# Kernel tuning notes

Measured on AMD Instinct MI355X. Metric: run time of the kernel, lower is better.

Reference implementation:

```python
import jax, jax.numpy as jnp
import numpy as np

H = 128  # GRU units / embedding dim


def gru_dir(x, mask, W, U, b):
    """Keras GRU (reset_after=True), return final state.
    x: [B,T,D] float, mask: [B,T] bool, W: [D,3H], U: [H,3H], b: [2,3H] (input/recurrent bias).
    Gate order in kernels: z, r, h (Keras convention).
    """
    bi, bh = b[0], b[1]
    xproj = jnp.einsum('btd,dk->btk', x, W) + bi          # [B,T,3H] precomputed input projection
    xproj_t = jnp.transpose(xproj, (1, 0, 2))             # [T,B,3H]
    mask_t = jnp.transpose(mask, (1, 0))                  # [T,B]
    h0 = jnp.zeros((x.shape[0], H), dtype=x.dtype)

    def step(h, inp):
        xp, m = inp                                       # [B,3H], [B]
        hU = h @ U + bh                                   # [B,3H]
        z = jax.nn.sigmoid(xp[:, :H] + hU[:, :H])
        r = jax.nn.sigmoid(xp[:, H:2 * H] + hU[:, H:2 * H])
        hh = jnp.tanh(xp[:, 2 * H:] + r * hU[:, 2 * H:])
        h_new = z * h + (1.0 - z) * hh
        h = jnp.where(m[:, None], h_new, h)               # masked steps carry state
        return h, None

    h_final, _ = jax.lax.scan(step, h0, (xproj_t, mask_t))
    return h_final                                        # [B,H]


def setup_inputs() -> dict:
    key = jax.random.key(0)
    ks = jax.random.split(key, 10)
    B, T, V = 512, 512, 50000
    tokens = jax.random.randint(ks[0], (B, T), 0, V, dtype=jnp.int32)
    s = 0.05
    emb = jax.random.normal(ks[1], (V, H), dtype=jnp.float32) * s
    Wf = jax.random.normal(ks[2], (H, 3 * H), dtype=jnp.float32) * s
    Uf = jax.random.normal(ks[3], (H, 3 * H), dtype=jnp.float32) * s
    bf = jnp.zeros((2, 3 * H), dtype=jnp.float32)
    Wb = jax.random.normal(ks[4], (H, 3 * H), dtype=jnp.float32) * s
    Ub = jax.random.normal(ks[5], (H, 3 * H), dtype=jnp.float32) * s
    bb = jnp.zeros((2, 3 * H), dtype=jnp.float32)
    Wd = jax.random.normal(ks[6], (2 * H, 1), dtype=jnp.float32) * s
    bd = jnp.zeros((1,), dtype=jnp.float32)
    return {"tokens": tokens, "emb": emb, "Wf": Wf, "Uf": Uf, "bf": bf,
            "Wb": Wb, "Ub": Ub, "bb": bb, "Wd": Wd, "bd": bd}


def reference(tokens, emb, Wf, Uf, bf, Wb, Ub, bb, Wd, bd):
    x = emb[tokens]                                       # [B,T,H] embedding lookup
    mask = jnp.any(x != 0.0, axis=-1)                     # Masking(mask_value=0)
    x = x * mask[..., None].astype(x.dtype)               # Masking zeroes masked steps
    h_fwd = gru_dir(x, mask, Wf, Uf, bf)                  # forward direction
    h_bwd = gru_dir(x[:, ::-1, :], mask[:, ::-1], Wb, Ub, bb)  # backward direction (reversed time)
    h = jnp.concatenate([h_fwd, h_bwd], axis=-1)          # [B,2H] concat merge
    return jax.nn.sigmoid(h @ Wd + bd)                    # [B,1]
```

## Files before the change

### kernel.cpp

```cpp
#include <hip/hip_runtime.h>

#define TLEN 512
#define HD 128
#define VOC 50000

typedef float fvec4 __attribute__((ext_vector_type(4)));
typedef int   ivec4 __attribute__((ext_vector_type(4)));
typedef int   ivec8 __attribute__((ext_vector_type(8)));

__device__ __forceinline__ float fsig(float a){
  return __builtin_amdgcn_rcpf(1.f + __builtin_amdgcn_exp2f(-1.44269504f * a));
}

__global__ void emb_cvt8(const float* __restrict__ emb, int* __restrict__ out, int n4){
  int i = blockIdx.x * blockDim.x + threadIdx.x;
  if (i < n4){
    float4 v = *(const float4*)(emb + (size_t)i * 4);
    int p = __builtin_amdgcn_cvt_pk_fp8_f32(16.f * v.x, 16.f * v.y, 0, 0);
    p     = __builtin_amdgcn_cvt_pk_fp8_f32(16.f * v.z, 16.f * v.w, p, 1);
    out[i] = p;
  }
}

__global__ __launch_bounds__(512, 2) void gru_scan(
    const int* __restrict__ tokens, const unsigned char* __restrict__ embq,
    const float* __restrict__ Wf, const float* __restrict__ Uf, const float* __restrict__ bfv,
    const float* __restrict__ Wb, const float* __restrict__ Ub, const float* __restrict__ bbv,
    float* __restrict__ hbuf)
{
  const int tid  = threadIdx.x;
  const int wid  = tid >> 6, lane = tid & 63;
  const int l15  = lane & 15, l4 = lane >> 4;
  const int dir  = blockIdx.x >> 7, grp = blockIdx.x & 127;
  const int c    = wid * 16 + l15;

  const float* __restrict__ W  = dir ? Wb : Wf;
  const float* __restrict__ U  = dir ? Ub : Uf;
  const float* __restrict__ bv = dir ? bbv : bfv;

  __shared__ __attribute__((aligned(16))) unsigned char hl[98304];

  auto pack8 = [&](const float* M, int col)->ivec8{
    ivec8 q;
#pragma unroll
    for (int w = 0; w < 8; ++w){
      const int k0 = l4 * 32 + w * 4;
      int v = __builtin_amdgcn_cvt_pk_fp8_f32(16.f*M[(k0+0)*384 + col], 16.f*M[(k0+1)*384 + col], 0, 0);
      q[w]  = __builtin_amdgcn_cvt_pk_fp8_f32(16.f*M[(k0+2)*384 + col], 16.f*M[(k0+3)*384 + col], v, 1);
    }
    return q;
  };
  const ivec8 Qz = pack8(U, c), Qr = pack8(U, 128 + c), Qh = pack8(U, 256 + c);
  const ivec8 Pz = pack8(W, c), Pr = pack8(W, 128 + c), Ph = pack8(W, 256 + c);

  const float bz = bv[c] + bv[384 + c];
  const float br = bv[128 + c] + bv[384 + 128 + c];
  const float bx = bv[256 + c];
  const float bu = bv[384 + 256 + c];
  const fvec4 ZF = {0.f,0.f,0.f,0.f};
#define SP4(b) ((fvec4){(b),(b),(b),(b)})

  for (int i = tid; i < 2048; i += 512) ((int*)hl)[i] = 0;
  float h0 = 0.f;

  const int  brow = l15 >> 2, srow = l15 & 3;
  const long tbx  = (long)(grp * 4 + brow) * TLEN;
  const int  tb0  = dir ? (TLEN - 1) : 0, tsg = dir ? -1 : 1;
  auto tix = [&](int t){ t = (t > TLEN - 1) ? (TLEN - 1) : t; return tb0 + tsg * t; };
#define XLD(tok) (*(const ivec8*)(embq + (size_t)(tok) * HD + l4 * 32))
#define MFS(A, B, C) __builtin_amdgcn_mfma_scale_f32_16x16x128_f8f6f4(A, B, C, 0, 0, 0, 0x7B7B7B7B, 0, 0x7B7B7B7B)

  fvec4 xZ, xR, xX;
  ivec8 xfa;
  {
    const int t0 = tokens[tbx + tix(srow)];
    ivec8 xf0 = XLD(t0);
    xZ = MFS(xf0, Pz, SP4(bz)); xR = MFS(xf0, Pr, SP4(br)); xX = MFS(xf0, Ph, SP4(bx));
    xfa = XLD(tokens[tbx + tix(4 + srow)]);
  }
  int tok2 = tokens[tbx + tix(8 + srow)];

  const int hrd = l15 * 144 + l4 * 32;
  const int wb  = (4 * l4) * 144 + c;

  __syncthreads();

#define STEP(S, P, XTRA) { \
    ivec4 alo = *(const ivec4*)&hl[(P) + hrd]; \
    ivec4 ahi = *(const ivec4*)&hl[(P) + hrd + 16]; \
    ivec8 af = __builtin_shufflevector(alo, ahi, 0,1,2,3,4,5,6,7); \
    fvec4 aZ = MFS(af, Qz, ZF); \
    fvec4 aR = MFS(af, Qr, ZF); \
    fvec4 aU = MFS(af, Qh, ZF); \
    float z = fsig(xZ[S] + aZ[0]); \
    float r = fsig(xR[S] + aR[0]); \
    float a = xX[S] + r * (aU[0] + bu); a = fmaxf(a, -30.f); \
    float y = __builtin_amdgcn_exp2f(-2.88539008f * a); \
    float th = (1.f - y) * __builtin_amdgcn_rcpf(1.f + y); \
    h0 = th + z * (h0 - th); \
    hl[((P) ^ 4096) + wb] = \
        (unsigned char)(__builtin_amdgcn_cvt_pk_fp8_f32(16.f * h0, 16.f * h0, 0, 0) & 0xff); \
    XTRA \
    asm volatile("s_waitcnt lgkmcnt(0)" ::: "memory"); \
    __builtin_amdgcn_s_barrier(); \
}

  for (int g = 0; g < 128; ++g){
    STEP(0, 0,    { })
    STEP(1, 4096, { })
    STEP(2, 0,    { })
    STEP(3, 4096, {
      xZ = MFS(xfa, Pz, SP4(bz)); xR = MFS(xfa, Pr, SP4(br)); xX = MFS(xfa, Ph, SP4(bx));
      xfa = XLD(tok2);
      tok2 = tokens[tbx + tix(4 * (g + 3) + srow)];
    })
  }
#undef STEP
#undef MFS
#undef XLD
#undef SP4

  hbuf[(size_t)(grp * 4 + l4) * 256 + dir * 128 + c] = h0;
}

__global__ void head_k(const float* __restrict__ hbuf, const float* __restrict__ Wd,
                       const float* __restrict__ bd, float* __restrict__ out){
  const int wid = threadIdx.x >> 6, lane = threadIdx.x & 63;
  const int b = blockIdx.x * 4 + wid;
  const float* hr = hbuf + (size_t)b * 256;
  float s = 0.f;
#pragma unroll
  for (int j = 0; j < 4; ++j){ const int k = j * 64 + lane; s += hr[k] * Wd[k]; }
#pragma unroll
  for (int off = 32; off > 0; off >>= 1) s += __shfl_down(s, off);
  if (lane == 0) out[b] = 1.f / (1.f + __expf(-(s + bd[0])));
}

extern "C" void kernel_launch(void* const* d_in, const int* in_sizes, int n_in,
                              void* d_out, int out_size, void* d_ws, size_t ws_size,
                              hipStream_t stream){
  const int*   tokens = (const int*)  d_in[0];
  const float* emb    = (const float*)d_in[1];
  const float* Wf     = (const float*)d_in[2];
  const float* Uf     = (const float*)d_in[3];
  const float* bf_    = (const float*)d_in[4];
  const float* Wb     = (const float*)d_in[5];
  const float* Ub     = (const float*)d_in[6];
  const float* bb_    = (const float*)d_in[7];
  const float* Wd     = (const float*)d_in[8];
  const float* bd     = (const float*)d_in[9];
  float* out = (float*)d_out;

  unsigned char* embq = (unsigned char*)d_ws;
  float* hbuf = (float*)((char*)d_ws + (size_t)VOC * HD);

  const int n4 = VOC * HD / 4;
  emb_cvt8<<<(n4 + 255) / 256, 256, 0, stream>>>(emb, (int*)embq, n4);
  gru_scan<<<256, 512, 0, stream>>>(tokens, embq, Wf, Uf, bf_, Wb, Ub, bb_, hbuf);
  head_k<<<128, 256, 0, stream>>>(hbuf, Wd, bd, out);
}
```

Before: 177.0 us.

## Double-buffer input projections and spread their MFMAs across recurrent steps

The input-projection MFMAs for the next group of four timesteps are now issued one per step, placed between the LDS load and the recurrent MFMAs, instead of three at once at the end of every fourth step. Ping-pong register sets (even/odd) let the next group be computed while the current one is consumed, with the loop unrolled by two groups. This is meant to shorten the serial critical path of the step that used to carry the extra work. The hidden state is also kept pre-scaled by 16, which removes a multiply before the fp8 conversion, at the cost of more live registers.

Result: faster. 170.7 us (-3.5%).

```diff
diff --git a/kernel.cpp b/kernel.cpp
--- a/kernel.cpp
+++ b/kernel.cpp
@@ -61,7 +61,7 @@
 #define SP4(b) ((fvec4){(b),(b),(b),(b)})
 
   for (int i = tid; i < 2048; i += 512) ((int*)hl)[i] = 0;
-  float h0 = 0.f;
+  float h16 = 0.f;
 
   const int  brow = l15 >> 2, srow = l15 & 3;
   const long tbx  = (long)(grp * 4 + brow) * TLEN;
@@ -70,12 +70,12 @@
 #define XLD(tok) (*(const ivec8*)(embq + (size_t)(tok) * HD + l4 * 32))
 #define MFS(A, B, C) __builtin_amdgcn_mfma_scale_f32_16x16x128_f8f6f4(A, B, C, 0, 0, 0, 0x7B7B7B7B, 0, 0x7B7B7B7B)
 
-  fvec4 xZ, xR, xX;
-  ivec8 xfa;
+  fvec4 eZ, eR, eX, oZ = ZF, oR = ZF, oX = ZF;
+  ivec8 xfa, xfb;
   {
     const int t0 = tokens[tbx + tix(srow)];
     ivec8 xf0 = XLD(t0);
-    xZ = MFS(xf0, Pz, SP4(bz)); xR = MFS(xf0, Pr, SP4(br)); xX = MFS(xf0, Ph, SP4(bx));
+    eZ = MFS(xf0, Pz, SP4(bz)); eR = MFS(xf0, Pr, SP4(br)); eX = MFS(xf0, Ph, SP4(bx));
     xfa = XLD(tokens[tbx + tix(4 + srow)]);
   }
   int tok2 = tokens[tbx + tix(8 + srow)];
@@ -85,42 +85,46 @@
 
   __syncthreads();
 
-#define STEP(S, P, XTRA) { \
-    ivec4 alo = *(const ivec4*)&hl[(P) + hrd]; \
-    ivec4 ahi = *(const ivec4*)&hl[(P) + hrd + 16]; \
-    ivec8 af = __builtin_shufflevector(alo, ahi, 0,1,2,3,4,5,6,7); \
+#define STEP(S, P, XZ, XR, XX, XTOP) { \
+    ivec8 af; \
+    *(ivec4*)&af       = *(const ivec4*)&hl[(P) + hrd]; \
+    *((ivec4*)&af + 1) = *(const ivec4*)&hl[(P) + hrd + 16]; \
+    XTOP \
     fvec4 aZ = MFS(af, Qz, ZF); \
     fvec4 aR = MFS(af, Qr, ZF); \
     fvec4 aU = MFS(af, Qh, ZF); \
-    float z = fsig(xZ[S] + aZ[0]); \
-    float r = fsig(xR[S] + aR[0]); \
-    float a = xX[S] + r * (aU[0] + bu); a = fmaxf(a, -30.f); \
+    float z = fsig(XZ[S] + aZ[0]); \
+    float r = fsig(XR[S] + aR[0]); \
+    float a = XX[S] + r * (aU[0] + bu); a = fmaxf(a, -30.f); \
     float y = __builtin_amdgcn_exp2f(-2.88539008f * a); \
-    float th = (1.f - y) * __builtin_amdgcn_rcpf(1.f + y); \
-    h0 = th + z * (h0 - th); \
+    float th16 = (16.f - 16.f * y) * __builtin_amdgcn_rcpf(1.f + y); \
+    h16 = th16 + z * (h16 - th16); \
     hl[((P) ^ 4096) + wb] = \
-        (unsigned char)(__builtin_amdgcn_cvt_pk_fp8_f32(16.f * h0, 16.f * h0, 0, 0) & 0xff); \
-    XTRA \
+        (unsigned char)(__builtin_amdgcn_cvt_pk_fp8_f32(h16, h16, 0, 0) & 0xff); \
     asm volatile("s_waitcnt lgkmcnt(0)" ::: "memory"); \
     __builtin_amdgcn_s_barrier(); \
 }
 
-  for (int g = 0; g < 128; ++g){
-    STEP(0, 0,    { })
-    STEP(1, 4096, { })
-    STEP(2, 0,    { })
-    STEP(3, 4096, {
-      xZ = MFS(xfa, Pz, SP4(bz)); xR = MFS(xfa, Pr, SP4(br)); xX = MFS(xfa, Ph, SP4(bx));
-      xfa = XLD(tok2);
-      tok2 = tokens[tbx + tix(4 * (g + 3) + srow)];
-    })
+  for (int g = 0; g < 128; g += 2){
+    STEP(0, 0,    eZ,eR,eX, { oZ = MFS(xfa, Pz, SP4(bz));
+                              xfb = XLD(tok2);
+                              tok2 = tokens[tbx + tix(4 * (g + 3) + srow)]; })
+    STEP(1, 4096, eZ,eR,eX, { oR = MFS(xfa, Pr, SP4(br)); })
+    STEP(2, 0,    eZ,eR,eX, { oX = MFS(xfa, Ph, SP4(bx)); })
+    STEP(3, 4096, eZ,eR,eX, { })
+    STEP(0, 0,    oZ,oR,oX, { eZ = MFS(xfb, Pz, SP4(bz));
+                              xfa = XLD(tok2);
+                              tok2 = tokens[tbx + tix(4 * (g + 4) + srow)]; })
+    STEP(1, 4096, oZ,oR,oX, { eR = MFS(xfb, Pr, SP4(br)); })
+    STEP(2, 0,    oZ,oR,oX, { eX = MFS(xfb, Ph, SP4(bx)); })
+    STEP(3, 4096, oZ,oR,oX, { })
   }
 #undef STEP
 #undef MFS
 #undef XLD
 #undef SP4
 
-  hbuf[(size_t)(grp * 4 + l4) * 256 + dir * 128 + c] = h0;
+  hbuf[(size_t)(grp * 4 + l4) * 256 + dir * 128 + c] = h16 * 0.0625f;
 }
 
 __global__ void head_k(const float* __restrict__ hbuf, const float* __restrict__ Wd,
```
